# Performance work log

Hardware: AMD Instinct MI355X
Metric: run time of the kernel (lower is better)

Reference implementation:

```python
import jax, jax.numpy as jnp
import numpy as np

T, G, K, N = 131072, 64, 1024, 512  # batch_sum, batch_count, k, n
M_MAX = 4096  # static upper bound on any group size (setup guarantees <= 3072)
PAD = 128     # tile alignment for padded offsets


def setup_inputs() -> dict:
    key = jax.random.key(0)
    k1, k2 = jax.random.split(key)
    a = jax.random.normal(k1, (T, K), dtype=jnp.float32)
    b = jax.random.normal(k2, (G, K, N), dtype=jnp.float32) / np.float32(np.sqrt(K))
    rng = np.random.default_rng(0)
    d = rng.integers(-1024, 1024, G // 2)
    deltas = np.concatenate([d, -d])
    rng.shuffle(deltas)
    sizes = (T // G) + deltas  # each in [1024, 3072], sums exactly to T
    offsets = np.concatenate([[0], np.cumsum(sizes)[:-1]])
    padded = ((sizes + PAD - 1) // PAD) * PAD
    padded_offsets = np.concatenate([[0], np.cumsum(padded)[:-1]])
    return {
        "a": a,
        "b": b,
        "batch_sizes": jnp.asarray(sizes, dtype=jnp.int32),
        "batch_offsets": jnp.asarray(offsets, dtype=jnp.int32),
        "batch_padded_offsets": jnp.asarray(padded_offsets, dtype=jnp.int32),
    }


def reference(a, b, batch_sizes, batch_offsets, batch_padded_offsets):
    # Grouped GEMM: for each group g, out[off_g : off_g+size_g] = a[rows] @ b[g].
    # jit-friendly: scan over groups with a fixed M_MAX window, mask invalid rows.
    T_, _ = a.shape
    n_out = b.shape[-1]
    iota = jnp.arange(M_MAX)

    def body(out, xs):
        off, size, bg = xs
        rows = jnp.clip(off + iota, 0, T_ - 1)          # [M_MAX]
        mask = iota < size                               # [M_MAX]
        a_g = jnp.where(mask[:, None], a[rows], 0.0)     # [M_MAX, K]
        y = a_g @ bg                                     # [M_MAX, N]
        out = out.at[rows].add(y)                        # masked rows add zeros
        return out, None

    out0 = jnp.zeros((T_, n_out), dtype=a.dtype)
    out, _ = jax.lax.scan(body, out0, (batch_offsets, batch_sizes, b))
    return out
```

## Files before the change

kernel.cpp:

```cpp
#include <hip/hip_runtime.h>
#include <hip/hip_bf16.h>
#include <stdint.h>

#define T_ROWS 131072
#define GCNT   64
#define KDIM   1024
#define NDIM   512
#define BM     256
#define BN     256
#define BK     64
#define KTILES (KDIM / BK)
#define MT_MAX 640
#define NBLK   (MT_MAX * 2)

typedef __attribute__((ext_vector_type(4))) float f32x4;
typedef __attribute__((ext_vector_type(8))) short s16x8;
typedef __attribute__((ext_vector_type(4))) short s16x4;
typedef __attribute__((address_space(3))) unsigned int lds_u32;
typedef const __attribute__((address_space(1))) unsigned int gbl_u32;

static __device__ __forceinline__ short f2bf(float f) {
  __hip_bfloat16 h = __float2bfloat16(f);
  return __builtin_bit_cast(short, h);
}

__global__ __launch_bounds__(256) void bt_kernel(const float* __restrict__ b,
                                                 char* __restrict__ bt) {
  __shared__ short lt[64 * 130];
  int bid = blockIdx.x;
  int kt = bid & 15, nt = (bid >> 4) & 3, g = bid >> 6;
  int t = threadIdx.x;
  const float* src = b + ((size_t)(g * KDIM + kt * BK)) * NDIM + nt * 128;
#pragma unroll
  for (int i = 0; i < 32; i++) {
    int idx = i * 256 + t;
    int kk = idx >> 7, nn = idx & 127;
    lt[kk * 130 + nn] = f2bf(src[(size_t)kk * NDIM + nn]);
  }
  __syncthreads();
  char* dst = bt + ((size_t)bid << 14);
#pragma unroll
  for (int j = 0; j < 4; j++) {
    int chunk = j * 256 + t;
    int n = chunk >> 3;
    int slot = (chunk & 7) ^ (n & 7);
    s16x8 v;
#pragma unroll
    for (int i = 0; i < 8; i++) v[i] = lt[(slot * 8 + i) * 130 + n];
    *(s16x8*)(dst + (size_t)chunk * 16) = v;
  }
}

__global__ __launch_bounds__(512, 2) void gemm8(
    const float* __restrict__ a, const char* __restrict__ bt,
    const int* __restrict__ sizes, const int* __restrict__ offs,
    float* __restrict__ out) {
  __shared__ __align__(16) short lds_a[2][BM * BK];
  __shared__ __align__(16) char lds_b[2][BN * BK * 2];

  int bid0 = blockIdx.x;
  int bid = (bid0 & 7) * (NBLK / 8) + (bid0 >> 3);
  int bn = bid & 1;
  int tm = bid >> 1;

  int g = -1, m_loc = 0, base = 0;
#pragma unroll
  for (int i = 0; i < GCNT; i++) {
    int ps = (sizes[i] + 127) & ~127;
    int tg = (ps + 255) >> 8;
    if (tm >= base && tm < base + tg) { g = i; m_loc = (tm - base) << 8; }
    base += tg;
  }
  if (g < 0) return;
  int size = sizes[g], off = offs[g], valid = size - m_loc;

  int t = threadIdx.x, lane = t & 63, wid = t >> 6;
  int wm = wid >> 2, wn = wid & 3, lr = lane & 15, q = lane >> 4;

  int r0 = t >> 4, c16 = t & 15;
  int aoff[8];
#pragma unroll
  for (int i = 0; i < 8; i++) {
    int row = off + m_loc + i * 32 + r0;
    if (row >= T_ROWS) row = T_ROWS - 1;
    aoff[i] = row * KDIM + c16 * 4;
  }
  int a_wbyte = r0 * 128 + (((c16 >> 1) ^ (r0 & 7)) << 4) + (c16 & 1) * 8;

  const char* btbase = bt + ((size_t)g << 20);

  f32x4 acc[8][4];
#pragma unroll
  for (int i = 0; i < 8; i++)
#pragma unroll
    for (int j = 0; j < 4; j++) acc[i][j] = (f32x4){0.f, 0.f, 0.f, 0.f};
  f32x4 va[8];
  s16x8 af[4], bf0[4], bf1[4];

  auto issueA = [&](int kt, int h) {
#pragma unroll
    for (int i = 0; i < 4; i++)
      va[h * 4 + i] = *(const f32x4*)(a + aoff[h * 4 + i] + kt * BK);
  };
  auto writeA = [&](int c) {
    char* db = (char*)lds_a[c] + a_wbyte;
#pragma unroll
    for (int i = 0; i < 8; i++) {
      s16x4 v;
#pragma unroll
      for (int e = 0; e < 4; e++) v[e] = f2bf(va[i][e]);
      *(s16x4*)(db + i * 4096) = v;
    }
  };
  auto issueB = [&](int kt, int c, int h) {
#pragma unroll
    for (int i = 0; i < 2; i++) {
      int wc = wid * 4 + h * 2 + i;
      int sub = wc >> 4;
      int cc = (wc & 15) * 64 + lane;
      const char* gsrc =
          btbase + (((size_t)((bn * 2 + sub) * 16 + kt)) << 14) + cc * 16;
      __builtin_amdgcn_global_load_lds(
          (gbl_u32*)gsrc, (lds_u32*)((char*)lds_b[c] + wc * 1024), 16, 0, 0);
    }
  };
  auto dsA = [&](int c, int half, int ks) {
#pragma unroll
    for (int i = 0; i < 4; i++) {
      int row = wm * 128 + (half * 4 + i) * 16 + lr;
      int slot = (ks * 4 + q) ^ (row & 7);
      af[i] = *(const s16x8*)((const char*)lds_a[c] + row * 128 + slot * 16);
    }
  };
  auto dsB = [&](int c, int ks, s16x8* bf) {
#pragma unroll
    for (int fn = 0; fn < 4; fn++) {
      int n = wn * 64 + fn * 16 + lr;
      int slot = (ks * 4 + q) ^ (n & 7);
      bf[fn] = *(const s16x8*)((const char*)lds_b[c] + (n >> 7) * 16384 +
                               (n & 127) * 128 + slot * 16);
    }
  };
  auto pbar = [&]() {
    __builtin_amdgcn_sched_barrier(0);
    __builtin_amdgcn_s_barrier();
  };
  auto mfmaQ = [&](const s16x8* bf, int fmb) {
    __builtin_amdgcn_s_setprio(1);
#pragma unroll
    for (int fm = 0; fm < 4; fm++)
#pragma unroll
      for (int fn = 0; fn < 4; fn++)
        acc[fmb + fm][fn] = __builtin_amdgcn_mfma_f32_16x16x32_bf16(
            af[fm], bf[fn], acc[fmb + fm][fn], 0, 0, 0);
    __builtin_amdgcn_s_setprio(0);
    __builtin_amdgcn_sched_barrier(0);
  };

  issueA(0, 0);
  issueA(0, 1);
  writeA(0);
  issueB(0, 0, 0);
  issueB(0, 0, 1);
  issueB(1, 1, 0);
  issueB(1, 1, 1);
  asm volatile("s_waitcnt vmcnt(4) lgkmcnt(0)" ::: "memory");
  __builtin_amdgcn_sched_barrier(0);
  __builtin_amdgcn_s_barrier();

  for (int kt = 0; kt < KTILES - 2; kt++) {
    int cur = kt & 1, nxt = cur ^ 1;
    dsA(cur, 0, 0);
    dsB(cur, 0, bf0);
    issueA(kt + 1, 0);
    pbar();
    mfmaQ(bf0, 0);
    __builtin_amdgcn_s_barrier();
    dsA(cur, 0, 1);
    dsB(cur, 1, bf1);
    issueA(kt + 1, 1);
    pbar();
    mfmaQ(bf1, 0);
    __builtin_amdgcn_s_barrier();
    dsA(cur, 1, 0);
    issueB(kt + 2, cur, 0);
    pbar();
    mfmaQ(bf0, 4);
    __builtin_amdgcn_s_barrier();
    dsA(cur, 1, 1);
    issueB(kt + 2, cur, 1);
    pbar();
    mfmaQ(bf1, 4);
    __builtin_amdgcn_s_barrier();
    writeA(nxt);
    asm volatile("s_waitcnt lgkmcnt(0)" ::: "memory");
    __builtin_amdgcn_sched_barrier(0);
    __builtin_amdgcn_s_barrier();
  }

  {
    dsA(0, 0, 0); dsB(0, 0, bf0); issueA(15, 0);
    pbar(); mfmaQ(bf0, 0); __builtin_amdgcn_s_barrier();
    dsA(0, 0, 1); dsB(0, 1, bf1); issueA(15, 1);
    pbar(); mfmaQ(bf1, 0); __builtin_amdgcn_s_barrier();
    dsA(0, 1, 0); pbar(); mfmaQ(bf0, 4); __builtin_amdgcn_s_barrier();
    dsA(0, 1, 1); pbar(); mfmaQ(bf1, 4); __builtin_amdgcn_s_barrier();
    writeA(1);
    asm volatile("s_waitcnt lgkmcnt(0)" ::: "memory");
    __builtin_amdgcn_sched_barrier(0);
    __builtin_amdgcn_s_barrier();
  }
  {
    dsA(1, 0, 0); dsB(1, 0, bf0); pbar(); mfmaQ(bf0, 0);
    __builtin_amdgcn_s_barrier();
    dsA(1, 0, 1); dsB(1, 1, bf1); pbar(); mfmaQ(bf1, 0);
    __builtin_amdgcn_s_barrier();
    dsA(1, 1, 0); pbar(); mfmaQ(bf0, 4);
    __builtin_amdgcn_s_barrier();
    dsA(1, 1, 1); pbar(); mfmaQ(bf1, 4);
  }

  size_t orow0 = (size_t)(off + m_loc);
#pragma unroll
  for (int fm = 0; fm < 8; fm++) {
#pragma unroll
    for (int j = 0; j < 4; j++) {
      int rm = wm * 128 + fm * 16 + q * 4 + j;
      if (rm < valid) {
        float* orow = out + (orow0 + rm) * NDIM + bn * BN + wn * 64 + lr;
#pragma unroll
        for (int fn = 0; fn < 4; fn++) orow[fn * 16] = acc[fm][fn][j];
      }
    }
  }
}

__global__ __launch_bounds__(512, 2) void gemm_fb(
    const float* __restrict__ a, const float* __restrict__ b,
    const int* __restrict__ sizes, const int* __restrict__ offs,
    float* __restrict__ out) {
  __shared__ __align__(16) short lds_a[2][BM * BK];
  __shared__ __align__(16) char lds_b[2][BN * BK * 2];

  int bid0 = blockIdx.x;
  int bid = (bid0 & 7) * (NBLK / 8) + (bid0 >> 3);
  int bn = bid & 1;
  int tm = bid >> 1;

  int g = -1, m_loc = 0, base = 0;
#pragma unroll
  for (int i = 0; i < GCNT; i++) {
    int ps = (sizes[i] + 127) & ~127;
    int tg = (ps + 255) >> 8;
    if (tm >= base && tm < base + tg) { g = i; m_loc = (tm - base) << 8; }
    base += tg;
  }
  if (g < 0) return;
  int size = sizes[g], off = offs[g], valid = size - m_loc;

  int t = threadIdx.x, lane = t & 63, wid = t >> 6;
  int wm = wid >> 2, wn = wid & 3, lr = lane & 15, q = lane >> 4;

  int r0 = t >> 4, c16 = t & 15;
  int aoff[8];
#pragma unroll
  for (int i = 0; i < 8; i++) {
    int row = off + m_loc + i * 32 + r0;
    if (row >= T_ROWS) row = T_ROWS - 1;
    aoff[i] = row * KDIM + c16 * 4;
  }
  int a_wbyte = r0 * 128 + (((c16 >> 1) ^ (r0 & 7)) << 4) + (c16 & 1) * 8;
  int fb_n = t >> 1, fb_kh = (t & 1) * 32;

  f32x4 acc[8][4];
#pragma unroll
  for (int i = 0; i < 8; i++)
#pragma unroll
    for (int j = 0; j < 4; j++) acc[i][j] = (f32x4){0.f, 0.f, 0.f, 0.f};
  f32x4 va[8];

  auto loadA = [&](int kt) {
#pragma unroll
    for (int i = 0; i < 8; i++) va[i] = *(const f32x4*)(a + aoff[i] + kt * BK);
  };
  auto writeA = [&](int c) {
    char* db = (char*)lds_a[c] + a_wbyte;
#pragma unroll
    for (int i = 0; i < 8; i++) {
      s16x4 v;
#pragma unroll
      for (int e = 0; e < 4; e++) v[e] = f2bf(va[i][e]);
      *(s16x4*)(db + i * 4096) = v;
    }
  };
  auto stageB = [&](int kt, int c) {
    const float* p = b + (size_t)g * KDIM * NDIM +
                     (size_t)(kt * BK + fb_kh) * NDIM + bn * BN + fb_n;
    float vals[32];
#pragma unroll
    for (int i = 0; i < 32; i++) vals[i] = p[(size_t)i * NDIM];
    int nn = fb_n & 127;
    char* lb = (char*)lds_b[c] + (fb_n >> 7) * 16384 + nn * 128;
#pragma unroll
    for (int i8 = 0; i8 < 4; i8++) {
      int slot = (fb_kh >> 3) + i8;
      s16x8 v;
#pragma unroll
      for (int e = 0; e < 8; e++) v[e] = f2bf(vals[i8 * 8 + e]);
      *(s16x8*)(lb + (((slot ^ (nn & 7))) << 4)) = v;
    }
  };
  auto compute = [&](int c) {
#pragma unroll
    for (int ks = 0; ks < 2; ks++) {
      s16x8 af[8], bfr[4];
#pragma unroll
      for (int fm = 0; fm < 8; fm++) {
        int row = wm * 128 + fm * 16 + lr;
        int slot = (ks * 4 + q) ^ (row & 7);
        af[fm] = *(const s16x8*)((const char*)lds_a[c] + row * 128 + slot * 16);
      }
#pragma unroll
      for (int fn = 0; fn < 4; fn++) {
        int n = wn * 64 + fn * 16 + lr;
        int slot = (ks * 4 + q) ^ (n & 7);
        bfr[fn] = *(const s16x8*)((const char*)lds_b[c] + (n >> 7) * 16384 +
                                  (n & 127) * 128 + slot * 16);
      }
#pragma unroll
      for (int fm = 0; fm < 8; fm++)
#pragma unroll
        for (int fn = 0; fn < 4; fn++)
          acc[fm][fn] = __builtin_amdgcn_mfma_f32_16x16x32_bf16(
              af[fm], bfr[fn], acc[fm][fn], 0, 0, 0);
    }
  };

  loadA(0);
  stageB(0, 0);
  writeA(0);
  __syncthreads();
  int cur = 0;
  for (int kt = 0; kt < KTILES; kt++) {
    if (kt + 1 < KTILES) loadA(kt + 1);
    compute(cur);
    if (kt + 1 < KTILES) {
      stageB(kt + 1, cur ^ 1);
      writeA(cur ^ 1);
      __syncthreads();
      cur ^= 1;
    }
  }
  size_t orow0 = (size_t)(off + m_loc);
#pragma unroll
  for (int fm = 0; fm < 8; fm++) {
#pragma unroll
    for (int j = 0; j < 4; j++) {
      int rm = wm * 128 + fm * 16 + q * 4 + j;
      if (rm < valid) {
        float* orow = out + (orow0 + rm) * NDIM + bn * BN + wn * 64 + lr;
#pragma unroll
        for (int fn = 0; fn < 4; fn++) orow[fn * 16] = acc[fm][fn][j];
      }
    }
  }
}

extern "C" void kernel_launch(void* const* d_in, const int* in_sizes, int n_in,
                              void* d_out, int out_size, void* d_ws,
                              size_t ws_size, hipStream_t stream) {
  const float* a = (const float*)d_in[0];
  const float* b = (const float*)d_in[1];
  const int* sizes = (const int*)d_in[2];
  const int* offs = (const int*)d_in[3];
  float* out = (float*)d_out;

  const size_t bt_bytes = (size_t)GCNT * KDIM * NDIM * 2;
  if (ws_size >= bt_bytes) {
    bt_kernel<<<GCNT * 64, 256, 0, stream>>>(b, (char*)d_ws);
    gemm8<<<NBLK, 512, 0, stream>>>(a, (const char*)d_ws, sizes, offs, out);
  } else {
    gemm_fb<<<NBLK, 512, 0, stream>>>(a, b, sizes, offs, out);
  }
}
```

Before: 351.3 us.

## Restructure A/B prefetch pipeline: A two tiles ahead, B one ahead, split A commit

Reorders the software pipeline so the fp32 A tile is loaded two K-tiles ahead into registers and converted to bf16 in two halves interleaved with MFMA phases, while B is loaded directly to LDS one tile ahead. This removes the separate end-of-iteration writeA phase and its extra barrier, hiding the A conversion and LDS writes behind compute. It adds an lgkmcnt wait inside every phase barrier and relies on exact vmcnt accounting, which may serialize LDS reads more or hold more registers live.

```diff
diff --git a/kernel.cpp b/kernel.cpp
--- a/kernel.cpp
+++ b/kernel.cpp
@@ -78,13 +78,15 @@
   int wm = wid >> 2, wn = wid & 3, lr = lane & 15, q = lane >> 4;
 
   int r0 = t >> 4, c16 = t & 15;
-  int aoff[8];
-#pragma unroll
-  for (int i = 0; i < 8; i++) {
-    int row = off + m_loc + i * 32 + r0;
-    if (row >= T_ROWS) row = T_ROWS - 1;
-    aoff[i] = row * KDIM + c16 * 4;
-  }
+  int aoff[2][4];
+#pragma unroll
+  for (int h = 0; h < 2; h++)
+#pragma unroll
+    for (int i = 0; i < 4; i++) {
+      int row = off + m_loc + h * 128 + i * 32 + r0;
+      if (row >= T_ROWS) row = T_ROWS - 1;
+      aoff[h][i] = row * KDIM + c16 * 4;
+    }
   int a_wbyte = r0 * 128 + (((c16 >> 1) ^ (r0 & 7)) << 4) + (c16 & 1) * 8;
 
   const char* btbase = bt + ((size_t)g << 20);
@@ -94,21 +96,21 @@
   for (int i = 0; i < 8; i++)
 #pragma unroll
     for (int j = 0; j < 4; j++) acc[i][j] = (f32x4){0.f, 0.f, 0.f, 0.f};
-  f32x4 va[8];
+  f32x4 va[2][4];
   s16x8 af[4], bf0[4], bf1[4];
 
   auto issueA = [&](int kt, int h) {
 #pragma unroll
     for (int i = 0; i < 4; i++)
-      va[h * 4 + i] = *(const f32x4*)(a + aoff[h * 4 + i] + kt * BK);
-  };
-  auto writeA = [&](int c) {
-    char* db = (char*)lds_a[c] + a_wbyte;
-#pragma unroll
-    for (int i = 0; i < 8; i++) {
+      va[h][i] = *(const f32x4*)(a + aoff[h][i] + kt * BK);
+  };
+  auto commitA = [&](int c, int h) {
+    char* db = (char*)lds_a[c] + h * 16384 + a_wbyte;
+#pragma unroll
+    for (int i = 0; i < 4; i++) {
       s16x4 v;
 #pragma unroll
-      for (int e = 0; e < 4; e++) v[e] = f2bf(va[i][e]);
+      for (int e = 0; e < 4; e++) v[e] = f2bf(va[h][i][e]);
       *(s16x4*)(db + i * 4096) = v;
     }
   };
@@ -144,6 +146,8 @@
   auto pbar = [&]() {
     __builtin_amdgcn_sched_barrier(0);
     __builtin_amdgcn_s_barrier();
+    asm volatile("s_waitcnt lgkmcnt(0)" ::: "memory");
+    __builtin_amdgcn_sched_barrier(0);
   };
   auto mfmaQ = [&](const s16x8* bf, int fmb) {
     __builtin_amdgcn_s_setprio(1);
@@ -157,14 +161,15 @@
     __builtin_amdgcn_sched_barrier(0);
   };
 
+  issueB(0, 0, 0);
+  issueB(0, 0, 1);
   issueA(0, 0);
   issueA(0, 1);
-  writeA(0);
-  issueB(0, 0, 0);
-  issueB(0, 0, 1);
-  issueB(1, 1, 0);
-  issueB(1, 1, 1);
-  asm volatile("s_waitcnt vmcnt(4) lgkmcnt(0)" ::: "memory");
+  commitA(0, 0);
+  commitA(0, 1);
+  issueA(1, 0);
+  issueA(1, 1);
+  asm volatile("s_waitcnt vmcnt(8) lgkmcnt(0)" ::: "memory");
   __builtin_amdgcn_sched_barrier(0);
   __builtin_amdgcn_s_barrier();
 
@@ -172,42 +177,45 @@
     int cur = kt & 1, nxt = cur ^ 1;
     dsA(cur, 0, 0);
     dsB(cur, 0, bf0);
-    issueA(kt + 1, 0);
+    issueB(kt + 1, nxt, 0);
     pbar();
     mfmaQ(bf0, 0);
     __builtin_amdgcn_s_barrier();
     dsA(cur, 0, 1);
     dsB(cur, 1, bf1);
-    issueA(kt + 1, 1);
+    issueB(kt + 1, nxt, 1);
     pbar();
     mfmaQ(bf1, 0);
     __builtin_amdgcn_s_barrier();
     dsA(cur, 1, 0);
-    issueB(kt + 2, cur, 0);
+    commitA(nxt, 0);
+    issueA(kt + 2, 0);
     pbar();
     mfmaQ(bf0, 4);
     __builtin_amdgcn_s_barrier();
     dsA(cur, 1, 1);
-    issueB(kt + 2, cur, 1);
-    pbar();
+    commitA(nxt, 1);
+    issueA(kt + 2, 1);
+    __builtin_amdgcn_sched_barrier(0);
+    asm volatile("s_waitcnt vmcnt(8) lgkmcnt(0)" ::: "memory");
+    __builtin_amdgcn_sched_barrier(0);
+    __builtin_amdgcn_s_barrier();
     mfmaQ(bf1, 4);
     __builtin_amdgcn_s_barrier();
-    writeA(nxt);
-    asm volatile("s_waitcnt lgkmcnt(0)" ::: "memory");
-    __builtin_amdgcn_sched_barrier(0);
-    __builtin_amdgcn_s_barrier();
   }
 
   {
-    dsA(0, 0, 0); dsB(0, 0, bf0); issueA(15, 0);
+    dsA(0, 0, 0); dsB(0, 0, bf0); issueB(15, 1, 0);
     pbar(); mfmaQ(bf0, 0); __builtin_amdgcn_s_barrier();
-    dsA(0, 0, 1); dsB(0, 1, bf1); issueA(15, 1);
+    dsA(0, 0, 1); dsB(0, 1, bf1); issueB(15, 1, 1);
     pbar(); mfmaQ(bf1, 0); __builtin_amdgcn_s_barrier();
-    dsA(0, 1, 0); pbar(); mfmaQ(bf0, 4); __builtin_amdgcn_s_barrier();
-    dsA(0, 1, 1); pbar(); mfmaQ(bf1, 4); __builtin_amdgcn_s_barrier();
-    writeA(1);
-    asm volatile("s_waitcnt lgkmcnt(0)" ::: "memory");
-    __builtin_amdgcn_sched_barrier(0);
+    dsA(0, 1, 0); commitA(1, 0);
+    pbar(); mfmaQ(bf0, 4); __builtin_amdgcn_s_barrier();
+    dsA(0, 1, 1); commitA(1, 1);
+    asm volatile("s_waitcnt vmcnt(0) lgkmcnt(0)" ::: "memory");
+    __builtin_amdgcn_sched_barrier(0);
+    __builtin_amdgcn_s_barrier();
+    mfmaQ(bf1, 4);
     __builtin_amdgcn_s_barrier();
   }
   {
```

New measurement: 325.1 us. 1.08x faster.
